# Kernel optimization log

Measured on AMD Instinct MI355X. Metric: run time of the kernel, lower is better.

Reference implementation:

```python
import jax, jax.numpy as jnp
import numpy as np

B, F, S, P, E, H = 64, 32, 512, 96, 8, 2048
TOP_K = 2
ALPHA = 10.0
ENT_EPS = 1e-8
CV_EPS = 1e-10


def setup_inputs() -> dict:
    key = jax.random.key(0)
    ks = jax.random.split(key, 8)
    s = 0.02
    return {
        "x": jax.random.normal(ks[0], (B, F, S), dtype=jnp.float32),
        "time_embedding": jax.random.normal(ks[1], (B, F, S), dtype=jnp.float32),
        "Wg": jax.random.normal(ks[2], (S, E), dtype=jnp.float32) * s,
        "bg": jnp.zeros((E,), dtype=jnp.float32),
        "W1": jax.random.normal(ks[3], (E, S, H), dtype=jnp.float32) * s,
        "b1": jnp.zeros((E, H), dtype=jnp.float32),
        "W2": jax.random.normal(ks[4], (E, H, P), dtype=jnp.float32) * s,
        "b2": jnp.zeros((E, P), dtype=jnp.float32),
    }


def _gates(tf, Wg, bg):
    # tf: [F, B, S] -> logits [F, B, E]
    logits = jnp.einsum('fbs,se->fbe', tf, Wg) + bg
    # kthvalue(x, E - top_k + 1) = (E - top_k)-th entry (0-based) of ascending sort = k-th largest
    kth = jnp.sort(logits, axis=-1)[..., E - TOP_K]  # [F, B]
    mask = logits < kth[..., None]
    sm = jax.nn.softmax(logits, axis=-1)
    dec = jnp.where(mask, ALPHA * jnp.log(sm + 1.0), ALPHA * (jnp.exp(sm) - 1.0))
    return jax.nn.softmax(dec, axis=-1)  # [F, B, E]


def reference(x, time_embedding, Wg, bg, W1, b1, W2, b2):
    xf = jnp.transpose(x, (1, 0, 2))               # [F, B, S]
    tf = jnp.transpose(time_embedding, (1, 0, 2))  # [F, B, S]
    gates = _gates(tf, Wg, bg)                     # [F, B, E]

    # all experts on all features (eval mode: dropout = identity)
    h = jax.nn.gelu(jnp.einsum('fbs,esh->febh', xf, W1) + b1[None, :, None, :], approximate=False)
    eo = jnp.einsum('febh,ehp->febp', h, W2) + b2[None, :, None, :]  # [F, E, B, P]
    out = jnp.einsum('fbe,febp->fbp', gates, eo)   # gated weighted sum
    output = jnp.transpose(out, (1, 0, 2))         # [B, F, P]

    # selector loss: cv_squared of importance = gates.sum(batch) expanded over pred_len
    gsum = gates.sum(axis=1)                       # [F, E]
    imp = jnp.broadcast_to(gsum[..., None], (F, E, P)).reshape(F, E * P)
    cv = jnp.var(imp, axis=1, ddof=1) / (jnp.mean(imp, axis=1) ** 2 + CV_EPS)
    selector_loss = jnp.sum(cv)                    # loss_coef = 1.0

    # entropy loss: importance1 = gates.mean(batch) expanded over pred_len
    gmean = gates.mean(axis=1)                     # [F, E]
    imp1 = jnp.broadcast_to(gmean[..., None], (F, E, P))
    entropy_loss = jnp.sum((-imp1 * jnp.log(imp1 + ENT_EPS)).mean(axis=(1, 2)))

    return output, selector_loss, entropy_loss
```

## Files before the change

### kernel.cpp

```cpp
#include <hip/hip_runtime.h>
#include <math.h>

#define B_ 64
#define F_ 32
#define S_ 512
#define P_ 96
#define E_ 8
#define H_ 2048
#define M_ 2048

#define BM 128
#define BH 128
#define BK 64
#define ZSPLIT 4
#define HPZ (H_ / ZSPLIT)
#define NHT (HPZ / BH)
#define NKC (S_ / BK)
#define HPITCH 136

typedef __bf16 bf16x8 __attribute__((ext_vector_type(8)));
typedef __bf16 bf16x4 __attribute__((ext_vector_type(4)));
typedef float f32x4 __attribute__((ext_vector_type(4)));

#define MFMA16(a, b, c) __builtin_amdgcn_mfma_f32_16x16x32_bf16((a), (b), (c), 0, 0, 0)

#define GLL16(gp, lp) __builtin_amdgcn_global_load_lds(                     \
    (const __attribute__((address_space(1))) void*)(gp),                    \
    (__attribute__((address_space(3))) void*)(lp), 16, 0, 0)

__device__ __forceinline__ float fast_gelu(float x) {
  float e = __builtin_amdgcn_exp2f(-2.45546696f * x);
  return x * __builtin_amdgcn_rcpf(1.0f + e);
}

#define PREP_GRID 3584

__global__ __launch_bounds__(256) void k_prep(const float* __restrict__ x,
                                              const float* __restrict__ te,
                                              const float* __restrict__ Wg,
                                              const float* __restrict__ bg,
                                              const float* __restrict__ W1,
                                              const float* __restrict__ W2,
                                              __bf16* __restrict__ xbf,
                                              __bf16* __restrict__ w1t,
                                              __bf16* __restrict__ w2t,
                                              float* __restrict__ gates) {
  __shared__ float tile[64 * 65];
  const int blk = blockIdx.x;
  const int tid = threadIdx.x;

  if (blk < 2048) {
    int e = blk >> 8, tt = blk & 255;
    int si = tt >> 5, hi = tt & 31;
    const float* src = W1 + (size_t)e * S_ * H_ + (size_t)(si * 64) * H_ + hi * 64;
    {
      int row = tid >> 2;
      int cb = (tid & 3) * 16;
#pragma unroll
      for (int k = 0; k < 4; ++k) {
        f32x4 v = *(const f32x4*)(src + (size_t)row * H_ + cb + k * 4);
#pragma unroll
        for (int u = 0; u < 4; ++u) tile[row * 65 + cb + k * 4 + u] = v[u];
      }
    }
    __syncthreads();
    {
      int h = tid >> 2;
      int sb = (tid & 3) * 16;
      __bf16* dst = w1t + (size_t)e * H_ * S_ + (size_t)(hi * 64 + h) * S_ + si * 64 + sb;
      bf16x8 o0, o1;
#pragma unroll
      for (int k = 0; k < 8; ++k) o0[k] = (__bf16)tile[(sb + k) * 65 + h];
#pragma unroll
      for (int k = 0; k < 8; ++k) o1[k] = (__bf16)tile[(sb + 8 + k) * 65 + h];
      *(bf16x8*)dst = o0;
      *(bf16x8*)(dst + 8) = o1;
    }
    return;
  }
  if (blk < 2560) {
    int t = blk - 2048;
    int e = t >> 6, hi = (t >> 1) & 31, ph = t & 1;
    const float* src = W2 + (size_t)e * H_ * P_ + (size_t)(hi * 64) * P_ + ph * 48;
    {
      int h = tid & 63;
      int seg = tid >> 6;
#pragma unroll
      for (int k = 0; k < 3; ++k) {
        f32x4 v = *(const f32x4*)(src + (size_t)h * P_ + seg * 12 + k * 4);
#pragma unroll
        for (int u = 0; u < 4; ++u) tile[h * 49 + seg * 12 + k * 4 + u] = v[u];
      }
    }
    __syncthreads();
    if (tid < 192) {
      int p = tid >> 2;
      int hb = (tid & 3) * 16;
      __bf16* dst = w2t + (size_t)e * P_ * H_ + (size_t)(ph * 48 + p) * H_ + hi * 64 + hb;
      bf16x8 o0, o1;
#pragma unroll
      for (int k = 0; k < 8; ++k) o0[k] = (__bf16)tile[(hb + k) * 49 + p];
#pragma unroll
      for (int k = 0; k < 8; ++k) o1[k] = (__bf16)tile[(hb + 8 + k) * 49 + p];
      *(bf16x8*)dst = o0;
      *(bf16x8*)(dst + 8) = o1;
    }
    return;
  }
  if (blk < 3072) {
    size_t i = (size_t)(blk - 2560) * 2048 + (size_t)tid * 8;
#pragma unroll
    for (int k = 0; k < 2; ++k) {
      f32x4 v = *(const f32x4*)(x + i + k * 4);
      bf16x4 o = {(__bf16)v[0], (__bf16)v[1], (__bf16)v[2], (__bf16)v[3]};
      *(bf16x4*)(xbf + i + k * 4) = o;
    }
    return;
  }
  int wave = tid >> 6, lane = tid & 63;
  int m = (blk - 3072) * 4 + wave;
  const float* trow = te + (size_t)m * S_;
  float acc[E_];
#pragma unroll
  for (int e = 0; e < E_; ++e) acc[e] = 0.f;
  for (int s = lane; s < S_; s += 64) {
    float t = trow[s];
    const f32x4* wgr = (const f32x4*)(Wg + s * E_);
    f32x4 a = wgr[0], b = wgr[1];
    acc[0] += t * a[0]; acc[1] += t * a[1]; acc[2] += t * a[2]; acc[3] += t * a[3];
    acc[4] += t * b[0]; acc[5] += t * b[1]; acc[6] += t * b[2]; acc[7] += t * b[3];
  }
#pragma unroll
  for (int e = 0; e < E_; ++e) {
#pragma unroll
    for (int off = 32; off > 0; off >>= 1) acc[e] += __shfl_xor(acc[e], off, 64);
  }
  if (lane == 0) {
    float lg[E_];
    float m1 = -3.4e38f, m2 = -3.4e38f;
#pragma unroll
    for (int e = 0; e < E_; ++e) {
      float v = acc[e] + bg[e];
      lg[e] = v;
      if (v > m1) { m2 = m1; m1 = v; }
      else if (v > m2) { m2 = v; }
    }
    float den = 0.f, sm[E_];
#pragma unroll
    for (int e = 0; e < E_; ++e) { sm[e] = expf(lg[e] - m1); den += sm[e]; }
    float inv = 1.f / den;
    float dmax = -3.4e38f, dec[E_];
#pragma unroll
    for (int e = 0; e < E_; ++e) {
      float p = sm[e] * inv;
      float d = (lg[e] < m2) ? (10.f * logf(p + 1.f)) : (10.f * (expf(p) - 1.f));
      dec[e] = d;
      dmax = fmaxf(dmax, d);
    }
    float dden = 0.f;
#pragma unroll
    for (int e = 0; e < E_; ++e) { dec[e] = expf(dec[e] - dmax); dden += dec[e]; }
    float dinv = 1.f / dden;
#pragma unroll
    for (int e = 0; e < E_; ++e) gates[m * E_ + e] = dec[e] * dinv;
  }
}

__global__ __launch_bounds__(256, 2) void k_experts(
    const __bf16* __restrict__ xbf,
    const __bf16* __restrict__ w1t,
    const __bf16* __restrict__ w2t,
    const float* __restrict__ b1,
    const float* __restrict__ b2,
    const float* __restrict__ gates,
    float* __restrict__ out)
{
  __shared__ __align__(16) __bf16 W1s[BH * BK];
  __shared__ __align__(16) __bf16 Xs[BM * BK];
  __shared__ __align__(16) __bf16 Hs[BM * HPITCH];

  const int tid = threadIdx.x;

  if (blockIdx.z == ZSPLIT) {
    if (blockIdx.x != 0 || blockIdx.y != 0) return;
    float* gsum = (float*)&Hs[0];
    float* cvs  = gsum + F_ * E_;
    float* ents = cvs + F_;
    int f = tid >> 3, e = tid & 7;
    float s = 0.f;
    for (int b = 0; b < B_; ++b) s += gates[(size_t)(b * F_ + f) * E_ + e];
    gsum[f * E_ + e] = s;
    __syncthreads();
    if (tid < F_) {
      float mean = 0.f;
#pragma unroll
      for (int k = 0; k < E_; ++k) mean += gsum[tid * E_ + k];
      mean *= (1.f / E_);
      float ss = 0.f;
#pragma unroll
      for (int k = 0; k < E_; ++k) { float d = gsum[tid * E_ + k] - mean; ss += d * d; }
      float var = (float)P_ * ss / (float)(E_ * P_ - 1);
      cvs[tid] = var / (mean * mean + 1e-10f);
      float ent = 0.f;
#pragma unroll
      for (int k = 0; k < E_; ++k) { float g = gsum[tid * E_ + k] * (1.f / B_); ent += -g * logf(g + 1e-8f); }
      ents[tid] = ent * (1.f / E_);
    }
    __syncthreads();
    if (tid == 0) {
      float a = 0.f, b = 0.f;
      for (int k = 0; k < F_; ++k) { a += cvs[k]; b += ents[k]; }
      out[(size_t)M_ * P_ + 0] = a;
      out[(size_t)M_ * P_ + 1] = b;
    }
    return;
  }

  const int wave = tid >> 6, lane = tid & 63;
  const int l15 = lane & 15, quad = lane >> 4;
  const int e = blockIdx.x;
  const int m0 = blockIdx.y * BM;
  const int hz = blockIdx.z * HPZ;

  const int sg = lane & 7;
  const int srl = lane >> 3;
  const int gcol = ((sg ^ srl) * 8);

  const __bf16* xg = xbf + (size_t)(m0 + wave * 8 + srl) * S_ + gcol;
  const __bf16* w1base = w1t + ((size_t)e * H_ + hz + wave * 8 + srl) * S_ + gcol;
  const __bf16* w2z = w2t + (size_t)e * P_ * H_ + hz;

  const int hq = (wave >> 1) * 64;
  const int mq = (wave & 1) * 64;
  const int w32 = wave * 32;

  const f32x4 fz = {0.f, 0.f, 0.f, 0.f};
  f32x4 acc2[2][6];
#pragma unroll
  for (int rt = 0; rt < 2; ++rt)
#pragma unroll
    for (int j = 0; j < 6; ++j) acc2[rt][j] = fz;

  for (int ht = 0; ht < NHT; ++ht) {
    const __bf16* w1g = w1base + (size_t)(ht * BH) * S_;
    f32x4 acc1[4][4];
#pragma unroll
    for (int i = 0; i < 4; ++i)
#pragma unroll
      for (int j = 0; j < 4; ++j) acc1[i][j] = fz;

    for (int kc = 0; kc < NKC; ++kc) {
#pragma unroll
      for (int p = 0; p < 4; ++p) {
        GLL16(w1g + (size_t)(p * 32) * S_ + kc * BK, &W1s[(p * 32 + wave * 8) * BK]);
        GLL16(xg  + (size_t)(p * 32) * S_ + kc * BK, &Xs[(p * 32 + wave * 8) * BK]);
      }
      __syncthreads();
#pragma unroll
      for (int kk = 0; kk < 2; ++kk) {
        bf16x8 a[4], b[4];
#pragma unroll
        for (int i = 0; i < 4; ++i) {
          int r = hq + i * 16 + l15;
          int g = kk * 4 + quad;
          a[i] = *(const bf16x8*)&W1s[r * BK + ((g ^ (r & 7)) * 8)];
        }
#pragma unroll
        for (int j = 0; j < 4; ++j) {
          int r = mq + j * 16 + l15;
          int g = kk * 4 + quad;
          b[j] = *(const bf16x8*)&Xs[r * BK + ((g ^ (r & 7)) * 8)];
        }
#pragma unroll
        for (int i = 0; i < 4; ++i)
#pragma unroll
          for (int j = 0; j < 4; ++j)
            acc1[i][j] = MFMA16(a[i], b[j], acc1[i][j]);
      }
      __syncthreads();
    }

    {
      const float* b1w = b1 + (size_t)e * H_ + hz + ht * BH + hq;
#pragma unroll
      for (int i = 0; i < 4; ++i) {
        f32x4 bv = *(const f32x4*)(b1w + i * 16 + quad * 4);
#pragma unroll
        for (int j = 0; j < 4; ++j) {
          bf16x4 hv;
#pragma unroll
          for (int r = 0; r < 4; ++r)
            hv[r] = (__bf16)fast_gelu(acc1[i][j][r] + bv[r]);
          *(bf16x4*)&Hs[(mq + j * 16 + l15) * HPITCH + hq + i * 16 + quad * 4] = hv;
        }
      }
    }
    __syncthreads();

    {
      const __bf16* w2c = w2z + ht * BH;
#pragma unroll
      for (int kk = 0; kk < 4; ++kk) {
        bf16x8 a0 = *(const bf16x8*)&Hs[(w32 + l15) * HPITCH + kk * 32 + quad * 8];
        bf16x8 a1 = *(const bf16x8*)&Hs[(w32 + 16 + l15) * HPITCH + kk * 32 + quad * 8];
#pragma unroll
        for (int j = 0; j < 6; ++j) {
          bf16x8 b = *(const bf16x8*)(w2c + (size_t)(j * 16 + l15) * H_ + kk * 32 + quad * 8);
          acc2[0][j] = MFMA16(a0, b, acc2[0][j]);
          acc2[1][j] = MFMA16(a1, b, acc2[1][j]);
        }
      }
    }
  }

#pragma unroll
  for (int rt = 0; rt < 2; ++rt) {
#pragma unroll
    for (int r = 0; r < 4; ++r) {
      int m = m0 + w32 + rt * 16 + quad * 4 + r;
      float g = gates[m * E_ + e];
#pragma unroll
      for (int j = 0; j < 6; ++j) {
        int col = j * 16 + l15;
        float v = acc2[rt][j][r];
        if (blockIdx.z == 0) v += b2[e * P_ + col];
        atomicAdd(&out[(size_t)m * P_ + col], g * v);
      }
    }
  }
}

extern "C" void kernel_launch(void* const* d_in, const int* in_sizes, int n_in,
                              void* d_out, int out_size, void* d_ws, size_t ws_size,
                              hipStream_t stream) {
  const float* x  = (const float*)d_in[0];
  const float* te = (const float*)d_in[1];
  const float* Wg = (const float*)d_in[2];
  const float* bg = (const float*)d_in[3];
  const float* W1 = (const float*)d_in[4];
  const float* b1 = (const float*)d_in[5];
  const float* W2 = (const float*)d_in[6];
  const float* b2 = (const float*)d_in[7];
  float* out = (float*)d_out;

  char* ws = (char*)d_ws;
  float* gates = (float*)ws;
  __bf16* xbf  = (__bf16*)(ws + 65536);
  __bf16* w1t  = (__bf16*)(ws + 65536 + 2097152);
  __bf16* w2t  = (__bf16*)(ws + 65536 + 2097152 + 16777216);

  hipMemsetAsync(d_out, 0, (size_t)out_size * sizeof(float), stream);
  k_prep<<<PREP_GRID, 256, 0, stream>>>(x, te, Wg, bg, W1, W2, xbf, w1t, w2t, gates);
  k_experts<<<dim3(E_, M_ / BM, ZSPLIT + 1), 256, 0, stream>>>(xbf, w1t, w2t, b1, b2, gates, out);
}
```

Measured before the change: 193.7 us.

## Restructure W1 transpose, fuse output zeroing into prep, alias LDS for occupancy

The W1 transpose is reorganised so each block handles a full 64-column strip over all S rows, converting to bf16 in LDS before transposing. This replaces many small blocks with fewer, larger ones. The output memset is folded into the prep kernel as extra zeroing blocks, which removes a separate launch. In the expert kernel the X tile now aliases the H staging buffer, with an added barrier, so LDS use drops and launch bounds can allow 3 blocks per CU. The added synchronisation and aliasing risk stalls and hazards, and the fewer prep blocks may lower memory parallelism.

```diff
diff --git a/kernel.cpp b/kernel.cpp
--- a/kernel.cpp
+++ b/kernel.cpp
@@ -33,7 +33,7 @@
   return x * __builtin_amdgcn_rcpf(1.0f + e);
 }
 
-#define PREP_GRID 3584
+#define PREP_GRID 1984
 
 __global__ __launch_bounds__(256) void k_prep(const float* __restrict__ x,
                                               const float* __restrict__ te,
@@ -44,42 +44,53 @@
                                               __bf16* __restrict__ xbf,
                                               __bf16* __restrict__ w1t,
                                               __bf16* __restrict__ w2t,
-                                              float* __restrict__ gates) {
-  __shared__ float tile[64 * 65];
+                                              float* __restrict__ gates,
+                                              float* __restrict__ out) {
+  __shared__ __align__(16) __bf16 btile[256 * 68];
   const int blk = blockIdx.x;
   const int tid = threadIdx.x;
 
-  if (blk < 2048) {
-    int e = blk >> 8, tt = blk & 255;
-    int si = tt >> 5, hi = tt & 31;
-    const float* src = W1 + (size_t)e * S_ * H_ + (size_t)(si * 64) * H_ + hi * 64;
-    {
-      int row = tid >> 2;
-      int cb = (tid & 3) * 16;
-#pragma unroll
-      for (int k = 0; k < 4; ++k) {
-        f32x4 v = *(const f32x4*)(src + (size_t)row * H_ + cb + k * 4);
-#pragma unroll
-        for (int u = 0; u < 4; ++u) tile[row * 65 + cb + k * 4 + u] = v[u];
-      }
-    }
-    __syncthreads();
-    {
-      int h = tid >> 2;
-      int sb = (tid & 3) * 16;
-      __bf16* dst = w1t + (size_t)e * H_ * S_ + (size_t)(hi * 64 + h) * S_ + si * 64 + sb;
-      bf16x8 o0, o1;
-#pragma unroll
-      for (int k = 0; k < 8; ++k) o0[k] = (__bf16)tile[(sb + k) * 65 + h];
-#pragma unroll
-      for (int k = 0; k < 8; ++k) o1[k] = (__bf16)tile[(sb + 8 + k) * 65 + h];
-      *(bf16x8*)dst = o0;
-      *(bf16x8*)(dst + 8) = o1;
-    }
-    return;
-  }
-  if (blk < 2560) {
-    int t = blk - 2048;
+  if (blk < 256) {
+    int e = blk >> 5, hstrip = blk & 31;
+    const float* src = W1 + (size_t)e * S_ * H_ + hstrip * 64;
+    __bf16* dstb = w1t + (size_t)e * H_ * S_ + (size_t)(hstrip * 64) * S_;
+#pragma unroll
+    for (int pass = 0; pass < 2; ++pass) {
+      {
+        int rb = tid >> 2;
+        int hseg = (tid & 3) * 16;
+#pragma unroll
+        for (int it = 0; it < 4; ++it) {
+          int r = it * 64 + rb;
+          const float* srow = src + (size_t)(pass * 256 + r) * H_ + hseg;
+#pragma unroll
+          for (int k = 0; k < 4; ++k) {
+            f32x4 v = *(const f32x4*)(srow + k * 4);
+            bf16x4 o = {(__bf16)v[0], (__bf16)v[1], (__bf16)v[2], (__bf16)v[3]};
+            *(bf16x4*)&btile[r * 68 + hseg + k * 4] = o;
+          }
+        }
+      }
+      __syncthreads();
+      {
+        int h = tid >> 2;
+        int sseg = (tid & 3) * 64;
+        __bf16* drow = dstb + (size_t)h * S_ + pass * 256 + sseg;
+#pragma unroll
+        for (int g = 0; g < 8; ++g) {
+          bf16x8 o;
+#pragma unroll
+          for (int j = 0; j < 8; ++j) o[j] = btile[(sseg + g * 8 + j) * 68 + h];
+          *(bf16x8*)(drow + g * 8) = o;
+        }
+      }
+      __syncthreads();
+    }
+    return;
+  }
+  if (blk < 768) {
+    float* tile = (float*)&btile[0];
+    int t = blk - 256;
     int e = t >> 6, hi = (t >> 1) & 31, ph = t & 1;
     const float* src = W2 + (size_t)e * H_ * P_ + (size_t)(hi * 64) * P_ + ph * 48;
     {
@@ -107,8 +118,8 @@
     }
     return;
   }
-  if (blk < 3072) {
-    size_t i = (size_t)(blk - 2560) * 2048 + (size_t)tid * 8;
+  if (blk < 1280) {
+    size_t i = (size_t)(blk - 768) * 2048 + (size_t)tid * 8;
 #pragma unroll
     for (int k = 0; k < 2; ++k) {
       f32x4 v = *(const f32x4*)(x + i + k * 4);
@@ -117,56 +128,64 @@
     }
     return;
   }
-  int wave = tid >> 6, lane = tid & 63;
-  int m = (blk - 3072) * 4 + wave;
-  const float* trow = te + (size_t)m * S_;
-  float acc[E_];
-#pragma unroll
-  for (int e = 0; e < E_; ++e) acc[e] = 0.f;
-  for (int s = lane; s < S_; s += 64) {
-    float t = trow[s];
-    const f32x4* wgr = (const f32x4*)(Wg + s * E_);
-    f32x4 a = wgr[0], b = wgr[1];
-    acc[0] += t * a[0]; acc[1] += t * a[1]; acc[2] += t * a[2]; acc[3] += t * a[3];
-    acc[4] += t * b[0]; acc[5] += t * b[1]; acc[6] += t * b[2]; acc[7] += t * b[3];
-  }
-#pragma unroll
-  for (int e = 0; e < E_; ++e) {
-#pragma unroll
-    for (int off = 32; off > 0; off >>= 1) acc[e] += __shfl_xor(acc[e], off, 64);
-  }
-  if (lane == 0) {
-    float lg[E_];
-    float m1 = -3.4e38f, m2 = -3.4e38f;
+  if (blk < 1792) {
+    int wave = tid >> 6, lane = tid & 63;
+    int m = (blk - 1280) * 4 + wave;
+    const float* trow = te + (size_t)m * S_;
+    float acc[E_];
+#pragma unroll
+    for (int e = 0; e < E_; ++e) acc[e] = 0.f;
+    for (int s = lane; s < S_; s += 64) {
+      float t = trow[s];
+      const f32x4* wgr = (const f32x4*)(Wg + s * E_);
+      f32x4 a = wgr[0], b = wgr[1];
+      acc[0] += t * a[0]; acc[1] += t * a[1]; acc[2] += t * a[2]; acc[3] += t * a[3];
+      acc[4] += t * b[0]; acc[5] += t * b[1]; acc[6] += t * b[2]; acc[7] += t * b[3];
+    }
 #pragma unroll
     for (int e = 0; e < E_; ++e) {
-      float v = acc[e] + bg[e];
-      lg[e] = v;
-      if (v > m1) { m2 = m1; m1 = v; }
-      else if (v > m2) { m2 = v; }
-    }
-    float den = 0.f, sm[E_];
-#pragma unroll
-    for (int e = 0; e < E_; ++e) { sm[e] = expf(lg[e] - m1); den += sm[e]; }
-    float inv = 1.f / den;
-    float dmax = -3.4e38f, dec[E_];
-#pragma unroll
-    for (int e = 0; e < E_; ++e) {
-      float p = sm[e] * inv;
-      float d = (lg[e] < m2) ? (10.f * logf(p + 1.f)) : (10.f * (expf(p) - 1.f));
-      dec[e] = d;
-      dmax = fmaxf(dmax, d);
-    }
-    float dden = 0.f;
-#pragma unroll
-    for (int e = 0; e < E_; ++e) { dec[e] = expf(dec[e] - dmax); dden += dec[e]; }
-    float dinv = 1.f / dden;
-#pragma unroll
-    for (int e = 0; e < E_; ++e) gates[m * E_ + e] = dec[e] * dinv;
+#pragma unroll
+      for (int off = 32; off > 0; off >>= 1) acc[e] += __shfl_xor(acc[e], off, 64);
+    }
+    if (lane == 0) {
+      float lg[E_];
+      float m1 = -3.4e38f, m2 = -3.4e38f;
+#pragma unroll
+      for (int e = 0; e < E_; ++e) {
+        float v = acc[e] + bg[e];
+        lg[e] = v;
+        if (v > m1) { m2 = m1; m1 = v; }
+        else if (v > m2) { m2 = v; }
+      }
+      float den = 0.f, sm[E_];
+#pragma unroll
+      for (int e = 0; e < E_; ++e) { sm[e] = expf(lg[e] - m1); den += sm[e]; }
+      float inv = 1.f / den;
+      float dmax = -3.4e38f, dec[E_];
+#pragma unroll
+      for (int e = 0; e < E_; ++e) {
+        float p = sm[e] * inv;
+        float d = (lg[e] < m2) ? (10.f * logf(p + 1.f)) : (10.f * (expf(p) - 1.f));
+        dec[e] = d;
+        dmax = fmaxf(dmax, d);
+      }
+      float dden = 0.f;
+#pragma unroll
+      for (int e = 0; e < E_; ++e) { dec[e] = expf(dec[e] - dmax); dden += dec[e]; }
+      float dinv = 1.f / dden;
+#pragma unroll
+      for (int e = 0; e < E_; ++e) gates[m * E_ + e] = dec[e] * dinv;
+    }
+    return;
+  }
+  {
+    size_t i = (size_t)(blk - 1792) * 1024 + (size_t)tid * 4;
+    f32x4 z = {0.f, 0.f, 0.f, 0.f};
+    *(f32x4*)(out + i) = z;
   }
 }
 
-__global__ __launch_bounds__(256, 2) void k_experts(
+__global__ __launch_bounds__(256, 3) void k_experts(
     const __bf16* __restrict__ xbf,
     const __bf16* __restrict__ w1t,
     const __bf16* __restrict__ w2t,
@@ -176,8 +195,9 @@
     float* __restrict__ out)
 {
   __shared__ __align__(16) __bf16 W1s[BH * BK];
-  __shared__ __align__(16) __bf16 Xs[BM * BK];
   __shared__ __align__(16) __bf16 Hs[BM * HPITCH];
+
+  __bf16* Xs = &Hs[0];
 
   const int tid = threadIdx.x;
 
@@ -311,6 +331,7 @@
         }
       }
     }
+    __syncthreads();
   }
 
 #pragma unroll
@@ -349,7 +370,6 @@
   __bf16* w1t  = (__bf16*)(ws + 65536 + 2097152);
   __bf16* w2t  = (__bf16*)(ws + 65536 + 2097152 + 16777216);
 
-  hipMemsetAsync(d_out, 0, (size_t)out_size * sizeof(float), stream);
-  k_prep<<<PREP_GRID, 256, 0, stream>>>(x, te, Wg, bg, W1, W2, xbf, w1t, w2t, gates);
+  k_prep<<<PREP_GRID, 256, 0, stream>>>(x, te, Wg, bg, W1, W2, xbf, w1t, w2t, gates, out);
   k_experts<<<dim3(E_, M_ / BM, ZSPLIT + 1), 256, 0, stream>>>(xbf, w1t, w2t, b1, b2, gates, out);
 }
```

Result: slower. 242.2 us (+25.0%).
